# Optimization experiments

Hardware: AMD Instinct MI355X
Metric: run time of the kernel (lower is better)

## Reference

```python
import jax, jax.numpy as jnp
import numpy as np

B, L, K, D, H = 2048, 1024, 128, 64, 4


def setup_inputs() -> dict:
    key = jax.random.key(0)
    ks = jax.random.split(key, 16)
    s = 1.0 / np.sqrt(D).astype(np.float32)  # keep softmax unsaturated
    return {
        "indices": jax.random.randint(ks[0], (B, K), 0, L),
        "user_seq_emb": jax.random.normal(ks[1], (B, L, D), jnp.float32),
        "target_emb": jax.random.normal(ks[2], (B, 1, D), jnp.float32),
        "WQ": jax.random.normal(ks[3], (H, D, D), jnp.float32) * s,
        "bQ": jax.random.normal(ks[4], (H, D), jnp.float32) * s,
        "WK": jax.random.normal(ks[5], (H, D, D), jnp.float32) * s,
        "bK": jax.random.normal(ks[6], (H, D), jnp.float32) * s,
        "WV": jax.random.normal(ks[7], (H, D, D), jnp.float32) * s,
        "bV": jax.random.normal(ks[8], (H, D), jnp.float32) * s,
        "WO": jax.random.normal(ks[9], (H * D, D), jnp.float32) * s,
        "bO": jax.random.normal(ks[10], (D,), jnp.float32) * s,
        "W1": jax.random.normal(ks[11], (2 * D, D), jnp.float32) * s,
        "b1": jax.random.normal(ks[12], (D,), jnp.float32) * s,
        "W2": jax.random.normal(ks[13], (D, 1), jnp.float32) * s,
        "b2": jax.random.normal(ks[14], (1,), jnp.float32) * s,
    }


def reference(indices, user_seq_emb, target_emb, WQ, bQ, WK, bK, WV, bV,
              WO, bO, W1, b1, W2, b2):
    d = user_seq_emb.shape[-1]
    # gather top-K history items: [B, K, D]
    topk = jnp.take_along_axis(user_seq_emb, indices[:, :, None], axis=1)
    # per-head projections, vectorized over heads (original loops in Python)
    q = jnp.einsum("bod,hde->bhoe", target_emb, WQ) + bQ[None, :, None, :]  # [B,H,1,D]
    k = jnp.einsum("bkd,hde->bhke", topk, WK) + bK[None, :, None, :]        # [B,H,K,D]
    v = jnp.einsum("bkd,hde->bhke", topk, WV) + bV[None, :, None, :]        # [B,H,K,D]
    scores = jnp.einsum("bhoe,bhke->bhk", q, k) / np.sqrt(d).astype(np.float32)
    attn = jax.nn.softmax(scores, axis=-1)                                   # [B,H,K]
    heads = jnp.einsum("bhk,bhke->bhe", attn, v)                             # [B,H,D]
    mhta = heads.reshape(heads.shape[0], -1) @ WO + bO                       # [B,D]
    # prediction layer: concat with target, MLP -> logit
    x = jnp.concatenate([mhta, target_emb[:, 0, :]], axis=-1)                # [B,2D]
    h = jax.nn.relu(x @ W1 + b1)
    logit = h @ W2 + b2                                                      # [B,1]
    return logit
```

## Files before the change

kernel.cpp:

```cpp
#include <hip/hip_runtime.h>

#define BB 2048
#define LL 1024
#define KK 128
#define DD 64
#define HH 4

__global__ __launch_bounds__(256) void fused_kernel(
    const int* __restrict__ idx, const float* __restrict__ seq,
    const float* __restrict__ tgt,
    const float* __restrict__ WQ, const float* __restrict__ bQ,
    const float* __restrict__ WK, const float* __restrict__ bK,
    const float* __restrict__ WV, const float* __restrict__ bV,
    const float* __restrict__ WO, const float* __restrict__ bO,
    const float* __restrict__ W1, const float* __restrict__ b1,
    const float* __restrict__ W2, const float* __restrict__ b2,
    float* __restrict__ outp)
{
    __shared__ float sTop[KK * 65];
    __shared__ float sT[DD];
    __shared__ float sA[256];
    __shared__ float sB[256];
    __shared__ float sSc[HH * KK];
    __shared__ float sCtx[256];
    __shared__ float sX[2 * DD];
    __shared__ float sSb[HH];

    const int t = threadIdx.x;
    const int b = blockIdx.x;
    const int h = t >> 6, e = t & 63;
    const int w = t >> 6, lane = t & 63;

    const int r0 = t >> 4;
    const int c0 = (t & 15) * 4;
    int rows[8];
    #pragma unroll
    for (int j = 0; j < 8; j++) rows[j] = idx[b * KK + r0 + 16 * j];
    float4 g[8];
    #pragma unroll
    for (int j = 0; j < 8; j++)
        g[j] = *(const float4*)(seq + ((size_t)b * LL + rows[j]) * DD + c0);

    if (t < DD) sT[t] = tgt[(size_t)b * DD + t];
    __syncthreads();

    float q = bQ[t];
    #pragma unroll 8
    for (int d = 0; d < DD; d++)
        q += sT[d] * WQ[((h << 6) + d) * 64 + e];
    sA[t] = q;

    {
        float p = q * bK[t];
        #pragma unroll
        for (int o = 32; o > 0; o >>= 1) p += __shfl_xor(p, o);
        if (e == 0) sSb[h] = p * 0.125f;
    }
    __syncthreads();

    {
        float acc2 = 0.f;
        const float* wrow = WK + (size_t)t * 64;
        #pragma unroll 4
        for (int i = 0; i < 64; i += 4) {
            float4 w4 = *(const float4*)(wrow + i);
            acc2 += w4.x * sA[(h << 6) + i]     + w4.y * sA[(h << 6) + i + 1]
                  + w4.z * sA[(h << 6) + i + 2] + w4.w * sA[(h << 6) + i + 3];
        }
        sB[t] = acc2 * 0.125f;
    }

    #pragma unroll
    for (int j = 0; j < 8; j++) {
        float* dst = &sTop[(r0 + 16 * j) * 65 + c0];
        dst[0] = g[j].x; dst[1] = g[j].y; dst[2] = g[j].z; dst[3] = g[j].w;
    }
    __syncthreads();

    #pragma unroll
    for (int s = 0; s < 2; s++) {
        int id = (s << 8) + t;
        int hh = id >> 7, k = id & 127;
        float a = 0.f;
        #pragma unroll 8
        for (int d = 0; d < DD; d++)
            a += sTop[k * 65 + d] * sB[(hh << 6) + d];
        sSc[(hh << 7) + k] = a + sSb[hh];
    }
    __syncthreads();

    {
        float x0 = sSc[(w << 7) + lane], x1 = sSc[(w << 7) + 64 + lane];
        float m = fmaxf(x0, x1);
        #pragma unroll
        for (int o = 32; o > 0; o >>= 1) m = fmaxf(m, __shfl_xor(m, o));
        float e0 = __expf(x0 - m), e1 = __expf(x1 - m);
        float s = e0 + e1;
        #pragma unroll
        for (int o = 32; o > 0; o >>= 1) s += __shfl_xor(s, o);
        float inv = 1.f / s;
        sSc[(w << 7) + lane] = e0 * inv;
        sSc[(w << 7) + 64 + lane] = e1 * inv;
    }
    __syncthreads();

    {
        float cacc = 0.f;
        #pragma unroll 8
        for (int k = 0; k < KK; k++)
            cacc += sSc[(w << 7) + k] * sTop[k * 65 + lane];
        sCtx[t] = cacc;
    }
    __syncthreads();

    {
        float hv = bV[t];
        #pragma unroll 8
        for (int d = 0; d < DD; d++)
            hv += sCtx[(h << 6) + d] * WV[((h << 6) + d) * 64 + e];
        sA[t] = hv;
    }
    __syncthreads();

    {
        float pa = 0.f;
        #pragma unroll 8
        for (int i = 0; i < 64; i++)
            pa += sA[(h << 6) + i] * WO[((h << 6) + i) * 64 + e];
        sB[t] = pa;
    }
    __syncthreads();

    if (t < 64) {
        sX[t] = sB[t] + sB[64 + t] + sB[128 + t] + sB[192 + t] + bO[t];
        sX[64 + t] = sT[t];
    }
    __syncthreads();

    {
        float a1 = 0.f;
        const int i0 = w << 5;
        #pragma unroll 8
        for (int i = i0; i < i0 + 32; i++)
            a1 += sX[i] * W1[i * 64 + lane];
        sB[(w << 6) + lane] = a1;
    }
    __syncthreads();
    if (t < 64) {
        float v = sB[t] + sB[64 + t] + sB[128 + t] + sB[192 + t] + b1[t];
        v = fmaxf(v, 0.f);
        float p = v * W2[t];
        #pragma unroll
        for (int o = 32; o > 0; o >>= 1) p += __shfl_xor(p, o);
        if (t == 0) outp[b] = p + b2[0];
    }
}

extern "C" void kernel_launch(void* const* d_in, const int* in_sizes, int n_in,
                              void* d_out, int out_size, void* d_ws, size_t ws_size,
                              hipStream_t stream)
{
    const int*   idx = (const int*)d_in[0];
    const float* seq = (const float*)d_in[1];
    const float* tgt = (const float*)d_in[2];
    const float* WQ  = (const float*)d_in[3];
    const float* bQ  = (const float*)d_in[4];
    const float* WK  = (const float*)d_in[5];
    const float* bK  = (const float*)d_in[6];
    const float* WV  = (const float*)d_in[7];
    const float* bV  = (const float*)d_in[8];
    const float* WO  = (const float*)d_in[9];
    const float* bO  = (const float*)d_in[10];
    const float* W1  = (const float*)d_in[11];
    const float* b1  = (const float*)d_in[12];
    const float* W2  = (const float*)d_in[13];
    const float* b2  = (const float*)d_in[14];
    float* outp = (float*)d_out;

    fused_kernel<<<dim3(BB), dim3(256), 0, stream>>>(
        idx, seq, tgt, WQ, bQ, WK, bK, WV, bV, WO, bO, W1, b1, W2, b2, outp);
}
```

Before: 648.6 us.

## Keep per-head vectors in registers via readlane and swizzle gathered tile in LDS

Each wave owns one head, so the intermediate vectors (q, folded key weights, scores, softmax weights, context, head outputs) are kept in registers and broadcast with readlane instead of being written to shared memory between barriers. This removes most __syncthreads and LDS round trips. The gathered top-K tile switches from padded scalar stores to an XOR-swizzled float4 layout so both the score and context passes can read it without bank conflicts. Launch bounds now also request 4 blocks per CU. Fully unrolled readlane loops add scalar instruction pressure and register use.

```diff
diff --git a/kernel.cpp b/kernel.cpp
--- a/kernel.cpp
+++ b/kernel.cpp
@@ -6,7 +6,11 @@
 #define DD 64
 #define HH 4
 
-__global__ __launch_bounds__(256) void fused_kernel(
+__device__ __forceinline__ float rl(float v, int l) {
+    return __int_as_float(__builtin_amdgcn_readlane(__float_as_int(v), l));
+}
+
+__global__ __launch_bounds__(256, 4) void fused_kernel(
     const int* __restrict__ idx, const float* __restrict__ seq,
     const float* __restrict__ tgt,
     const float* __restrict__ WQ, const float* __restrict__ bQ,
@@ -17,22 +21,16 @@
     const float* __restrict__ W2, const float* __restrict__ b2,
     float* __restrict__ outp)
 {
-    __shared__ float sTop[KK * 65];
-    __shared__ float sT[DD];
-    __shared__ float sA[256];
-    __shared__ float sB[256];
-    __shared__ float sSc[HH * KK];
-    __shared__ float sCtx[256];
+    __shared__ float sTop[KK * 64];
+    __shared__ float sP[256];
     __shared__ float sX[2 * DD];
-    __shared__ float sSb[HH];
 
     const int t = threadIdx.x;
     const int b = blockIdx.x;
-    const int h = t >> 6, e = t & 63;
     const int w = t >> 6, lane = t & 63;
 
     const int r0 = t >> 4;
-    const int c0 = (t & 15) * 4;
+    const int c0 = (t & 15) << 2;
     int rows[8];
     #pragma unroll
     for (int j = 0; j < 8; j++) rows[j] = idx[b * KK + r0 + 16 * j];
@@ -41,118 +39,114 @@
     for (int j = 0; j < 8; j++)
         g[j] = *(const float4*)(seq + ((size_t)b * LL + rows[j]) * DD + c0);
 
-    if (t < DD) sT[t] = tgt[(size_t)b * DD + t];
-    __syncthreads();
+    const float tg = tgt[(size_t)b * DD + lane];
 
     float q = bQ[t];
-    #pragma unroll 8
+    #pragma unroll
     for (int d = 0; d < DD; d++)
-        q += sT[d] * WQ[((h << 6) + d) * 64 + e];
-    sA[t] = q;
+        q += rl(tg, d) * WQ[((w << 6) + d) * 64 + lane];
 
+    float p = q * bK[t];
+    #pragma unroll
+    for (int o = 32; o > 0; o >>= 1) p += __shfl_xor(p, o);
+    const float sb = p * 0.125f;
+
+    float wk = 0.f;
     {
-        float p = q * bK[t];
+        const float* wrow = WK + (size_t)t * 64;
         #pragma unroll
-        for (int o = 32; o > 0; o >>= 1) p += __shfl_xor(p, o);
-        if (e == 0) sSb[h] = p * 0.125f;
-    }
-    __syncthreads();
-
-    {
-        float acc2 = 0.f;
-        const float* wrow = WK + (size_t)t * 64;
-        #pragma unroll 4
-        for (int i = 0; i < 64; i += 4) {
-            float4 w4 = *(const float4*)(wrow + i);
-            acc2 += w4.x * sA[(h << 6) + i]     + w4.y * sA[(h << 6) + i + 1]
-                  + w4.z * sA[(h << 6) + i + 2] + w4.w * sA[(h << 6) + i + 3];
+        for (int i = 0; i < 16; i++) {
+            float4 w4 = *(const float4*)(wrow + 4 * i);
+            wk += w4.x * rl(q, 4 * i)     + w4.y * rl(q, 4 * i + 1)
+                + w4.z * rl(q, 4 * i + 2) + w4.w * rl(q, 4 * i + 3);
         }
-        sB[t] = acc2 * 0.125f;
+        wk *= 0.125f;
     }
 
     #pragma unroll
     for (int j = 0; j < 8; j++) {
-        float* dst = &sTop[(r0 + 16 * j) * 65 + c0];
-        dst[0] = g[j].x; dst[1] = g[j].y; dst[2] = g[j].z; dst[3] = g[j].w;
+        int r = r0 + 16 * j;
+        *(float4*)&sTop[(r << 6) + (((c0 >> 2) ^ (r & 7)) << 2)] = g[j];
     }
     __syncthreads();
 
+    float acc0 = 0.f, acc1 = 0.f;
+    {
+        const int ra = lane << 6;
+        const int rb = (64 + lane) << 6;
+        const int rx = lane & 7;
+        #pragma unroll
+        for (int i = 0; i < 16; i++) {
+            const float4 va = *(const float4*)&sTop[ra + ((i ^ rx) << 2)];
+            const float4 vb = *(const float4*)&sTop[rb + ((i ^ rx) << 2)];
+            const float s0 = rl(wk, 4 * i),     s1 = rl(wk, 4 * i + 1);
+            const float s2 = rl(wk, 4 * i + 2), s3 = rl(wk, 4 * i + 3);
+            acc0 += s0 * va.x + s1 * va.y + s2 * va.z + s3 * va.w;
+            acc1 += s0 * vb.x + s1 * vb.y + s2 * vb.z + s3 * vb.w;
+        }
+    }
+    const float x0 = acc0 + sb, x1 = acc1 + sb;
+
+    float m = fmaxf(x0, x1);
     #pragma unroll
-    for (int s = 0; s < 2; s++) {
-        int id = (s << 8) + t;
-        int hh = id >> 7, k = id & 127;
-        float a = 0.f;
-        #pragma unroll 8
-        for (int d = 0; d < DD; d++)
-            a += sTop[k * 65 + d] * sB[(hh << 6) + d];
-        sSc[(hh << 7) + k] = a + sSb[hh];
+    for (int o = 32; o > 0; o >>= 1) m = fmaxf(m, __shfl_xor(m, o));
+    const float e0 = __expf(x0 - m), e1 = __expf(x1 - m);
+    float sden = e0 + e1;
+    #pragma unroll
+    for (int o = 32; o > 0; o >>= 1) sden += __shfl_xor(sden, o);
+    const float inv = 1.f / sden;
+    const float a0 = e0 * inv, a1 = e1 * inv;
+
+    float ctx = 0.f;
+    {
+        int cbase[8];
+        #pragma unroll
+        for (int c = 0; c < 8; c++)
+            cbase[c] = ((((lane >> 2) ^ c) << 2) + (lane & 3));
+        #pragma unroll
+        for (int k = 0; k < KK; k++) {
+            const float ak = (k < 64) ? rl(a0, k) : rl(a1, k - 64);
+            ctx += ak * sTop[(k << 6) + cbase[k & 7]];
+        }
     }
+
+    float hv = bV[t];
+    #pragma unroll
+    for (int d = 0; d < DD; d++)
+        hv += rl(ctx, d) * WV[((w << 6) + d) * 64 + lane];
+
+    float pa = 0.f;
+    #pragma unroll
+    for (int i = 0; i < DD; i++)
+        pa += rl(hv, i) * WO[((w << 6) + i) * 64 + lane];
+    sP[t] = pa;
+    __syncthreads();
+
+    if (t < 64)
+        sX[t] = sP[t] + sP[64 + t] + sP[128 + t] + sP[192 + t] + bO[t];
+    else if (t < 128)
+        sX[64 + (t - 64)] = tg;
     __syncthreads();
 
     {
-        float x0 = sSc[(w << 7) + lane], x1 = sSc[(w << 7) + 64 + lane];
-        float m = fmaxf(x0, x1);
+        float acc = 0.f;
+        const int i0 = w << 5;
         #pragma unroll
-        for (int o = 32; o > 0; o >>= 1) m = fmaxf(m, __shfl_xor(m, o));
-        float e0 = __expf(x0 - m), e1 = __expf(x1 - m);
-        float s = e0 + e1;
-        #pragma unroll
-        for (int o = 32; o > 0; o >>= 1) s += __shfl_xor(s, o);
-        float inv = 1.f / s;
-        sSc[(w << 7) + lane] = e0 * inv;
-        sSc[(w << 7) + 64 + lane] = e1 * inv;
-    }
-    __syncthreads();
-
-    {
-        float cacc = 0.f;
-        #pragma unroll 8
-        for (int k = 0; k < KK; k++)
-            cacc += sSc[(w << 7) + k] * sTop[k * 65 + lane];
-        sCtx[t] = cacc;
-    }
-    __syncthreads();
-
-    {
-        float hv = bV[t];
-        #pragma unroll 8
-        for (int d = 0; d < DD; d++)
-            hv += sCtx[(h << 6) + d] * WV[((h << 6) + d) * 64 + e];
-        sA[t] = hv;
-    }
-    __syncthreads();
-
-    {
-        float pa = 0.f;
-        #pragma unroll 8
-        for (int i = 0; i < 64; i++)
-            pa += sA[(h << 6) + i] * WO[((h << 6) + i) * 64 + e];
-        sB[t] = pa;
+        for (int ii = 0; ii < 32; ii++) {
+            const int i = i0 + ii;
+            acc += sX[i] * W1[i * 64 + lane];
+        }
+        sP[t] = acc;
     }
     __syncthreads();
 
     if (t < 64) {
-        sX[t] = sB[t] + sB[64 + t] + sB[128 + t] + sB[192 + t] + bO[t];
-        sX[64 + t] = sT[t];
-    }
-    __syncthreads();
-
-    {
-        float a1 = 0.f;
-        const int i0 = w << 5;
-        #pragma unroll 8
-        for (int i = i0; i < i0 + 32; i++)
-            a1 += sX[i] * W1[i * 64 + lane];
-        sB[(w << 6) + lane] = a1;
-    }
-    __syncthreads();
-    if (t < 64) {
-        float v = sB[t] + sB[64 + t] + sB[128 + t] + sB[192 + t] + b1[t];
+        float v = sP[t] + sP[64 + t] + sP[128 + t] + sP[192 + t] + b1[t];
         v = fmaxf(v, 0.f);
-        float p = v * W2[t];
+        float pp = v * W2[t];
         #pragma unroll
-        for (int o = 32; o > 0; o >>= 1) p += __shfl_xor(p, o);
-        if (t == 0) outp[b] = p + b2[0];
+        for (int o = 32; o > 0; o >>= 1) pp += __shfl_xor(pp, o);
+        if (t == 0) outp[b] = pp + b2[0];
     }
 }
 
```

After: 633.0 us. -2.4%, faster.
